# Kernel tuning notes

Hardware: AMD Instinct MI355X
Metric: run time of the kernel (lower is better)

Reference implementation:

```python
import jax, jax.numpy as jnp
import numpy as np

N_NODES = 200000
N_FRAGS = 50000
N_EDGES = 400000
HDIM = 128
VOCAB = 800


def setup_inputs() -> dict:
    key = jax.random.key(0)
    ks = jax.random.split(key, 9)
    x = jax.random.normal(ks[0], (N_NODES, HDIM), dtype=jnp.float32)
    fragments = jax.random.uniform(ks[1], (N_FRAGS, VOCAB), dtype=jnp.float32)
    emb_table = jax.random.normal(ks[2], (VOCAB, HDIM), dtype=jnp.float32)
    W_f = jax.random.normal(ks[3], (HDIM, HDIM), dtype=jnp.float32) / np.sqrt(HDIM)
    b_f = jax.random.normal(ks[4], (HDIM,), dtype=jnp.float32) * 0.01
    W_s = jax.random.normal(ks[5], (2 * HDIM, HDIM), dtype=jnp.float32) / np.sqrt(2 * HDIM)
    b_s = jax.random.normal(ks[6], (HDIM,), dtype=jnp.float32) * 0.01
    row = jax.random.randint(ks[7], (N_EDGES,), 0, N_NODES, dtype=jnp.int32)
    col = jax.random.randint(ks[8], (N_EDGES,), 0, N_FRAGS, dtype=jnp.int32)
    return {"x": x, "fragments": fragments, "emb_table": emb_table,
            "W_f": W_f, "b_f": b_f, "W_s": W_s, "b_s": b_s,
            "row": row, "col": col}


def _scatter_mean(vals, idx, num_segments):
    s = jax.ops.segment_sum(vals, idx, num_segments=num_segments)
    cnt = jax.ops.segment_sum(jnp.ones((vals.shape[0], 1), vals.dtype), idx,
                              num_segments=num_segments)
    return s / jnp.maximum(cnt, 1.0)


def reference(x, fragments, emb_table, W_f, b_f, W_s, b_s, row, col):
    N, H = x.shape
    F = fragments.shape[0]
    # gather node feats along memberships, mean-pool per fragment: [F, H]
    substructure_x = _scatter_mean(x[row], col, F)
    # fragment type embedding branch
    frag_ids = jnp.argmax(fragments, axis=1)            # [F]
    fragments_emb = emb_table[frag_ids] @ W_f + b_f      # [F, H]
    substructure_x = jnp.concatenate([substructure_x, fragments_emb], axis=1)  # [F, 2H]
    fragment_emb = substructure_x @ W_s + b_s            # [F, H]
    # gather fragment embeddings back to memberships, mean-pool per node: [N, H]
    return _scatter_mean(fragment_emb[col], row, N)
```

## Files before the change

### kernel.cpp

```cpp
#include <hip/hip_runtime.h>

#define HDIM 128
#define VOCAB 800
#define FB 16
#define TILE 1024

#define ACC4(a, v) { a.x += v.x; a.y += v.y; a.z += v.z; a.w += v.w; }

__global__ void k_prep(const float* __restrict__ emb, const float* __restrict__ W_f,
                       const float* __restrict__ W_s, const float* __restrict__ b_f,
                       const float* __restrict__ b_s, float* __restrict__ E2,
                       float* __restrict__ bfs) {
    __shared__ float e[HDIM], t1[HDIM];
    int j = threadIdx.x;
    int v = blockIdx.x;
    if (v < VOCAB) {
        e[j] = emb[(size_t)v * HDIM + j];
        __syncthreads();
        float a = 0.f;
        for (int k = 0; k < HDIM; ++k)
            a = fmaf(e[k], W_f[k * HDIM + j], a);
        t1[j] = a;
        __syncthreads();
        float b = 0.f;
        for (int k = 0; k < HDIM; ++k)
            b = fmaf(t1[k], W_s[(HDIM + k) * HDIM + j], b);
        E2[(size_t)v * HDIM + j] = b;
    } else {
        e[j] = b_f[j];
        __syncthreads();
        float b = b_s[j];
        for (int k = 0; k < HDIM; ++k)
            b = fmaf(e[k], W_s[(HDIM + k) * HDIM + j], b);
        bfs[j] = b;
    }
}

__global__ void k_amc(const float* __restrict__ frags, int* __restrict__ frag_id,
                      const int* __restrict__ row, const int* __restrict__ col,
                      int* __restrict__ cntr, int* __restrict__ cntc) {
    int b = blockIdx.x;
    if (b < 12500) {
        int wave = b * 4 + (threadIdx.x >> 6);
        int lane = threadIdx.x & 63;
        const float4* r = reinterpret_cast<const float4*>(frags + (size_t)wave * VOCAB);
        float best = -1e30f;
        int bidx = 0;
        for (int i = lane; i < VOCAB / 4; i += 64) {
            float4 v = r[i];
            int base = i * 4;
            if (v.x > best) { best = v.x; bidx = base + 0; }
            if (v.y > best) { best = v.y; bidx = base + 1; }
            if (v.z > best) { best = v.z; bidx = base + 2; }
            if (v.w > best) { best = v.w; bidx = base + 3; }
        }
        for (int off = 32; off > 0; off >>= 1) {
            float ov = __shfl_xor(best, off, 64);
            int   oi = __shfl_xor(bidx, off, 64);
            if (ov > best || (ov == best && oi < bidx)) { best = ov; bidx = oi; }
        }
        if (lane == 0) frag_id[wave] = bidx;
    } else {
        int i = (b - 12500) * 256 + threadIdx.x;
        if (i < 100000) {
            int4 r4 = reinterpret_cast<const int4*>(row)[i];
            int4 c4 = reinterpret_cast<const int4*>(col)[i];
            atomicAdd(&cntr[r4.x], 1); atomicAdd(&cntr[r4.y], 1);
            atomicAdd(&cntr[r4.z], 1); atomicAdd(&cntr[r4.w], 1);
            atomicAdd(&cntc[c4.x], 1); atomicAdd(&cntc[c4.y], 1);
            atomicAdd(&cntc[c4.z], 1); atomicAdd(&cntc[c4.w], 1);
        }
    }
}

__global__ void k_bsum2(const int* __restrict__ cntc, const int* __restrict__ cntr,
                        int* __restrict__ bsc, int* __restrict__ bsr, int NBC, int F, int N) {
    __shared__ int s[256];
    int t = threadIdx.x;
    const int* cnt;
    int* bsum;
    int bb, L;
    if ((int)blockIdx.x < NBC) { cnt = cntc; bsum = bsc; bb = blockIdx.x; L = F; }
    else                       { cnt = cntr; bsum = bsr; bb = blockIdx.x - NBC; L = N; }
    int i = bb * 256 + t;
    s[t] = (i < L) ? cnt[i] : 0;
    __syncthreads();
    for (int o = 128; o > 0; o >>= 1) {
        if (t < o) s[t] += s[t + o];
        __syncthreads();
    }
    if (t == 0) bsum[bb] = s[0];
}

__global__ void k_scan2(int* __restrict__ bsc, int* __restrict__ bsr, int nbc, int nbr) {
    __shared__ int s[1024];
    int* bsum = (blockIdx.x == 0) ? bsc : bsr;
    int nb    = (blockIdx.x == 0) ? nbc : nbr;
    int t = threadIdx.x;
    int v = (t < nb) ? bsum[t] : 0;
    s[t] = v;
    __syncthreads();
    for (int o = 1; o < 1024; o <<= 1) {
        int a = (t >= o) ? s[t - o] : 0;
        __syncthreads();
        s[t] += a;
        __syncthreads();
    }
    if (t < nb) bsum[t] = s[t] - v;
}

__global__ void k_base2(const int* __restrict__ cntc, const int* __restrict__ cntr,
                        const int* __restrict__ bsc, const int* __restrict__ bsr,
                        int* __restrict__ basec, int* __restrict__ baser,
                        int NBC, int F, int N) {
    __shared__ int s[256];
    int t = threadIdx.x;
    const int *cnt, *bsum;
    int* base;
    int bb, L;
    if ((int)blockIdx.x < NBC) { cnt = cntc; bsum = bsc; base = basec; bb = blockIdx.x; L = F; }
    else                       { cnt = cntr; bsum = bsr; base = baser; bb = blockIdx.x - NBC; L = N; }
    int i = bb * 256 + t;
    int v = (i < L) ? cnt[i] : 0;
    s[t] = v;
    __syncthreads();
    for (int o = 1; o < 256; o <<= 1) {
        int a = (t >= o) ? s[t - o] : 0;
        __syncthreads();
        s[t] += a;
        __syncthreads();
    }
    if (i < L) base[i] = bsum[bb] + s[t] - v;
}

__global__ void k_place(const int* __restrict__ row, const int* __restrict__ col,
                        const int* __restrict__ basec, const int* __restrict__ baser,
                        int* __restrict__ curc, int* __restrict__ curr,
                        int* __restrict__ payc, int* __restrict__ payr, int E) {
    int e = blockIdx.x * 256 + threadIdx.x;
    if (e >= E) return;
    int r = row[e], c = col[e];
    int pc = atomicAdd(&curc[c], 1);
    payc[basec[c] + pc] = r;
    int pr = atomicAdd(&curr[r], 1);
    payr[baser[r] + pr] = c;
}

__global__ __launch_bounds__(256) void k_frag(
        const float* __restrict__ x, const int* __restrict__ basec,
        const int* __restrict__ cntc, const int* __restrict__ payc,
        const int* __restrict__ frag_id, const float* __restrict__ W_s,
        const float* __restrict__ E2, const float* __restrict__ bfs,
        float* __restrict__ femb) {
    __shared__ float s[FB][HDIM];
    __shared__ int eidx[TILE];
    int t = threadIdx.x;
    int g = t >> 5, l = t & 31;
    int fb = blockIdx.x * FB;
    int fi0 = fb + g, fi1 = fb + 8 + g;
    int st0 = basec[fi0], d0 = cntc[fi0];
    int st1 = basec[fi1], d1 = cntc[fi1];
    int p0 = basec[fb];
    int pend = basec[fb + FB - 1] + cntc[fb + FB - 1];
    const float4* x4 = reinterpret_cast<const float4*>(x);
    float4 a0A = make_float4(0.f, 0.f, 0.f, 0.f), a0B = a0A, a1A = a0A, a1B = a0A;
    for (int tb = p0; tb < pend; tb += TILE) {
        int nload = min(TILE, pend - tb);
        for (int i = t; i < nload; i += 256) eidx[i] = payc[tb + i];
        __syncthreads();
        int lim = tb + nload;
        int lo0 = max(st0, tb) - tb, hi0 = min(st0 + d0, lim) - tb;
        int lo1 = max(st1, tb) - tb, hi1 = min(st1 + d1, lim) - tb;
        int m = max(hi0 - lo0, hi1 - lo1);
        for (int j = 0; j < m; j += 2) {
            if (lo0 + j < hi0)     { float4 v = x4[(size_t)eidx[lo0 + j]     * 32 + l]; ACC4(a0A, v); }
            if (lo0 + j + 1 < hi0) { float4 v = x4[(size_t)eidx[lo0 + j + 1] * 32 + l]; ACC4(a0B, v); }
            if (lo1 + j < hi1)     { float4 v = x4[(size_t)eidx[lo1 + j]     * 32 + l]; ACC4(a1A, v); }
            if (lo1 + j + 1 < hi1) { float4 v = x4[(size_t)eidx[lo1 + j + 1] * 32 + l]; ACC4(a1B, v); }
        }
        __syncthreads();
    }
    float inv0 = 1.0f / fmaxf((float)d0, 1.0f);
    float inv1 = 1.0f / fmaxf((float)d1, 1.0f);
    float4 r0, r1;
    r0.x = (a0A.x + a0B.x) * inv0; r0.y = (a0A.y + a0B.y) * inv0;
    r0.z = (a0A.z + a0B.z) * inv0; r0.w = (a0A.w + a0B.w) * inv0;
    r1.x = (a1A.x + a1B.x) * inv1; r1.y = (a1A.y + a1B.y) * inv1;
    r1.z = (a1A.z + a1B.z) * inv1; r1.w = (a1A.w + a1B.w) * inv1;
    *reinterpret_cast<float4*>(&s[g][l * 4]) = r0;
    *reinterpret_cast<float4*>(&s[8 + g][l * 4]) = r1;
    __syncthreads();
    int d = t & 127;
    int fh = t >> 7;
    float bv = bfs[d];
    float acc[8];
#pragma unroll
    for (int f = 0; f < 8; ++f)
        acc[f] = E2[(size_t)frag_id[fb + fh * 8 + f] * HDIM + d] + bv;
    for (int k = 0; k < HDIM; k += 4) {
        float w0 = W_s[(k + 0) * HDIM + d];
        float w1 = W_s[(k + 1) * HDIM + d];
        float w2 = W_s[(k + 2) * HDIM + d];
        float w3 = W_s[(k + 3) * HDIM + d];
#pragma unroll
        for (int f = 0; f < 8; ++f) {
            const float4 sv = *reinterpret_cast<const float4*>(&s[fh * 8 + f][k]);
            acc[f] = fmaf(sv.x, w0, acc[f]);
            acc[f] = fmaf(sv.y, w1, acc[f]);
            acc[f] = fmaf(sv.z, w2, acc[f]);
            acc[f] = fmaf(sv.w, w3, acc[f]);
        }
    }
#pragma unroll
    for (int f = 0; f < 8; ++f)
        femb[(size_t)(fb + fh * 8 + f) * HDIM + d] = acc[f];
}

__global__ __launch_bounds__(256) void k_node(
        const float* __restrict__ femb, const int* __restrict__ baser,
        const int* __restrict__ cntr, const int* __restrict__ payr,
        float* __restrict__ out, int N) {
    __shared__ int eidx[TILE];
    int t = threadIdx.x;
    int g = t >> 5, l = t & 31;
    int n0 = blockIdx.x * 32;
    int ng = n0 + g * 4;
    int p0 = baser[n0];
    int pend = baser[n0 + 31] + cntr[n0 + 31];
    int st0 = baser[ng + 0], d0 = cntr[ng + 0];
    int st1 = baser[ng + 1], d1 = cntr[ng + 1];
    int st2 = baser[ng + 2], d2 = cntr[ng + 2];
    int st3 = baser[ng + 3], d3 = cntr[ng + 3];
    const float4* f4 = reinterpret_cast<const float4*>(femb);
    float4 z = make_float4(0.f, 0.f, 0.f, 0.f);
    float4 a0A = z, a0B = z, a1A = z, a1B = z, a2A = z, a2B = z, a3A = z, a3B = z;
    for (int tb = p0; tb < pend; tb += TILE) {
        int nload = min(TILE, pend - tb);
        for (int i = t; i < nload; i += 256) eidx[i] = payr[tb + i];
        __syncthreads();
        int lim = tb + nload;
        int lo0 = max(st0, tb) - tb, hi0 = min(st0 + d0, lim) - tb;
        int lo1 = max(st1, tb) - tb, hi1 = min(st1 + d1, lim) - tb;
        int lo2 = max(st2, tb) - tb, hi2 = min(st2 + d2, lim) - tb;
        int lo3 = max(st3, tb) - tb, hi3 = min(st3 + d3, lim) - tb;
        int m = max(max(hi0 - lo0, hi1 - lo1), max(hi2 - lo2, hi3 - lo3));
        for (int j = 0; j < m; j += 2) {
            if (lo0 + j < hi0)     { float4 v = f4[(size_t)eidx[lo0 + j]     * 32 + l]; ACC4(a0A, v); }
            if (lo0 + j + 1 < hi0) { float4 v = f4[(size_t)eidx[lo0 + j + 1] * 32 + l]; ACC4(a0B, v); }
            if (lo1 + j < hi1)     { float4 v = f4[(size_t)eidx[lo1 + j]     * 32 + l]; ACC4(a1A, v); }
            if (lo1 + j + 1 < hi1) { float4 v = f4[(size_t)eidx[lo1 + j + 1] * 32 + l]; ACC4(a1B, v); }
            if (lo2 + j < hi2)     { float4 v = f4[(size_t)eidx[lo2 + j]     * 32 + l]; ACC4(a2A, v); }
            if (lo2 + j + 1 < hi2) { float4 v = f4[(size_t)eidx[lo2 + j + 1] * 32 + l]; ACC4(a2B, v); }
            if (lo3 + j < hi3)     { float4 v = f4[(size_t)eidx[lo3 + j]     * 32 + l]; ACC4(a3A, v); }
            if (lo3 + j + 1 < hi3) { float4 v = f4[(size_t)eidx[lo3 + j + 1] * 32 + l]; ACC4(a3B, v); }
        }
        __syncthreads();
    }
    float4* o4 = reinterpret_cast<float4*>(out);
    float4 r;
    float inv;
    inv = 1.0f / fmaxf((float)d0, 1.0f);
    r.x = (a0A.x + a0B.x) * inv; r.y = (a0A.y + a0B.y) * inv;
    r.z = (a0A.z + a0B.z) * inv; r.w = (a0A.w + a0B.w) * inv;
    o4[(size_t)(ng + 0) * 32 + l] = r;
    inv = 1.0f / fmaxf((float)d1, 1.0f);
    r.x = (a1A.x + a1B.x) * inv; r.y = (a1A.y + a1B.y) * inv;
    r.z = (a1A.z + a1B.z) * inv; r.w = (a1A.w + a1B.w) * inv;
    o4[(size_t)(ng + 1) * 32 + l] = r;
    inv = 1.0f / fmaxf((float)d2, 1.0f);
    r.x = (a2A.x + a2B.x) * inv; r.y = (a2A.y + a2B.y) * inv;
    r.z = (a2A.z + a2B.z) * inv; r.w = (a2A.w + a2B.w) * inv;
    o4[(size_t)(ng + 2) * 32 + l] = r;
    inv = 1.0f / fmaxf((float)d3, 1.0f);
    r.x = (a3A.x + a3B.x) * inv; r.y = (a3A.y + a3B.y) * inv;
    r.z = (a3A.z + a3B.z) * inv; r.w = (a3A.w + a3B.w) * inv;
    o4[(size_t)(ng + 3) * 32 + l] = r;
}

extern "C" void kernel_launch(void* const* d_in, const int* in_sizes, int n_in,
                              void* d_out, int out_size, void* d_ws, size_t ws_size,
                              hipStream_t stream) {
    const float* x         = (const float*)d_in[0];
    const float* fragments = (const float*)d_in[1];
    const float* emb_table = (const float*)d_in[2];
    const float* W_f       = (const float*)d_in[3];
    const float* b_f       = (const float*)d_in[4];
    const float* W_s       = (const float*)d_in[5];
    const float* b_s       = (const float*)d_in[6];
    const int*   row       = (const int*)d_in[7];
    const int*   col       = (const int*)d_in[8];
    float* out = (float*)d_out;

    const int N = 200000, F = 50000, E = 400000;
    const int NBC = (F + 255) / 256;
    const int NBR = (N + 255) / 256;

    float* femb   = (float*)d_ws;
    int* cntc     = (int*)(femb + (size_t)F * HDIM);
    int* cntr     = cntc + F;
    int* curc     = cntr + N;
    int* curr     = curc + F;
    int* basec    = curr + N;
    int* baser    = basec + F;
    int* bsc      = baser + N;
    int* bsr      = bsc + 1024;
    int* payc     = bsr + 1024;
    int* payr     = payc + E;
    int* frag_id  = payr + E;
    float* E2     = (float*)(frag_id + F);
    float* bfs    = E2 + VOCAB * HDIM;

    hipMemsetAsync(cntc, 0, (size_t)(2 * (F + N)) * sizeof(int), stream);

    k_prep<<<VOCAB + 1, HDIM, 0, stream>>>(emb_table, W_f, W_s, b_f, b_s, E2, bfs);
    k_amc<<<12500 + 391, 256, 0, stream>>>(fragments, frag_id, row, col, cntr, cntc);
    k_bsum2<<<NBC + NBR, 256, 0, stream>>>(cntc, cntr, bsc, bsr, NBC, F, N);
    k_scan2<<<2, 1024, 0, stream>>>(bsc, bsr, NBC, NBR);
    k_base2<<<NBC + NBR, 256, 0, stream>>>(cntc, cntr, bsc, bsr, basec, baser, NBC, F, N);
    k_place<<<(E + 255) / 256, 256, 0, stream>>>(row, col, basec, baser, curc, curr,
                                                 payc, payr, E);
    k_frag<<<F / FB, 256, 0, stream>>>(x, basec, cntc, payc, frag_id, W_s, E2, bfs, femb);
    k_node<<<N / 32, 256, 0, stream>>>(femb, baser, cntr, payr, out, N);
}
```

Baseline: 265.5 us.

## Gather bf16 copies of node and fragment features; fuse argmax into fragment kernel

Converts x to bf16 into the output buffer as scratch, and stores fragment embeddings as bf16, so both gather phases read half the bytes per row. The fragment-type argmax moves out of the counting kernel and into k_frag, where each 32-lane group computes it directly. k_node now handles 64 nodes per block with 8 accumulators per group and a smaller index tile. This cuts gather bandwidth at the cost of an extra full pass over x for conversion and bf16 rounding error in the results.

```diff
diff --git a/kernel.cpp b/kernel.cpp
--- a/kernel.cpp
+++ b/kernel.cpp
@@ -4,8 +4,18 @@
 #define VOCAB 800
 #define FB 16
 #define TILE 1024
-
-#define ACC4(a, v) { a.x += v.x; a.y += v.y; a.z += v.z; a.w += v.w; }
+#define TILE_N 512
+
+#define ACCB(a, h) { \
+    a.x += __uint_as_float(h.x << 16); \
+    a.y += __uint_as_float(h.x & 0xffff0000u); \
+    a.z += __uint_as_float(h.y << 16); \
+    a.w += __uint_as_float(h.y & 0xffff0000u); }
+
+static __device__ __forceinline__ unsigned short f2bf(float f) {
+    unsigned int u = __float_as_uint(f);
+    return (unsigned short)((u + 0x7fffu + ((u >> 16) & 1u)) >> 16);
+}
 
 __global__ void k_prep(const float* __restrict__ emb, const float* __restrict__ W_f,
                        const float* __restrict__ W_s, const float* __restrict__ b_f,
@@ -36,32 +46,22 @@
     }
 }
 
-__global__ void k_amc(const float* __restrict__ frags, int* __restrict__ frag_id,
+__global__ void k_cvt(const float* __restrict__ x, unsigned short* __restrict__ xb,
                       const int* __restrict__ row, const int* __restrict__ col,
                       int* __restrict__ cntr, int* __restrict__ cntc) {
-    int b = blockIdx.x;
+    int b = blockIdx.x, t = threadIdx.x;
     if (b < 12500) {
-        int wave = b * 4 + (threadIdx.x >> 6);
-        int lane = threadIdx.x & 63;
-        const float4* r = reinterpret_cast<const float4*>(frags + (size_t)wave * VOCAB);
-        float best = -1e30f;
-        int bidx = 0;
-        for (int i = lane; i < VOCAB / 4; i += 64) {
-            float4 v = r[i];
-            int base = i * 4;
-            if (v.x > best) { best = v.x; bidx = base + 0; }
-            if (v.y > best) { best = v.y; bidx = base + 1; }
-            if (v.z > best) { best = v.z; bidx = base + 2; }
-            if (v.w > best) { best = v.w; bidx = base + 3; }
-        }
-        for (int off = 32; off > 0; off >>= 1) {
-            float ov = __shfl_xor(best, off, 64);
-            int   oi = __shfl_xor(bidx, off, 64);
-            if (ov > best || (ov == best && oi < bidx)) { best = ov; bidx = oi; }
-        }
-        if (lane == 0) frag_id[wave] = bidx;
+        size_t i = ((size_t)b * 256 + t) * 8;
+        float4 v0 = *reinterpret_cast<const float4*>(x + i);
+        float4 v1 = *reinterpret_cast<const float4*>(x + i + 4);
+        uint4 o;
+        o.x = (unsigned)f2bf(v0.x) | ((unsigned)f2bf(v0.y) << 16);
+        o.y = (unsigned)f2bf(v0.z) | ((unsigned)f2bf(v0.w) << 16);
+        o.z = (unsigned)f2bf(v1.x) | ((unsigned)f2bf(v1.y) << 16);
+        o.w = (unsigned)f2bf(v1.z) | ((unsigned)f2bf(v1.w) << 16);
+        *reinterpret_cast<uint4*>(xb + i) = o;
     } else {
-        int i = (b - 12500) * 256 + threadIdx.x;
+        int i = (b - 12500) * 256 + t;
         if (i < 100000) {
             int4 r4 = reinterpret_cast<const int4*>(row)[i];
             int4 c4 = reinterpret_cast<const int4*>(col)[i];
@@ -147,22 +147,44 @@
 }
 
 __global__ __launch_bounds__(256) void k_frag(
-        const float* __restrict__ x, const int* __restrict__ basec,
-        const int* __restrict__ cntc, const int* __restrict__ payc,
-        const int* __restrict__ frag_id, const float* __restrict__ W_s,
+        const unsigned short* __restrict__ xb, const float* __restrict__ frags,
+        const int* __restrict__ basec, const int* __restrict__ cntc,
+        const int* __restrict__ payc, const float* __restrict__ W_s,
         const float* __restrict__ E2, const float* __restrict__ bfs,
-        float* __restrict__ femb) {
+        unsigned short* __restrict__ fembb) {
     __shared__ float s[FB][HDIM];
     __shared__ int eidx[TILE];
+    __shared__ int fidv[FB];
     int t = threadIdx.x;
     int g = t >> 5, l = t & 31;
     int fb = blockIdx.x * FB;
+#pragma unroll
+    for (int rep = 0; rep < 2; ++rep) {
+        int f = rep * 8 + g;
+        const float4* r = reinterpret_cast<const float4*>(frags + (size_t)(fb + f) * VOCAB);
+        float best = -1e30f;
+        int bidx = 0;
+        for (int i = l; i < VOCAB / 4; i += 32) {
+            float4 v = r[i];
+            int bI = i * 4;
+            if (v.x > best) { best = v.x; bidx = bI + 0; }
+            if (v.y > best) { best = v.y; bidx = bI + 1; }
+            if (v.z > best) { best = v.z; bidx = bI + 2; }
+            if (v.w > best) { best = v.w; bidx = bI + 3; }
+        }
+        for (int off = 16; off > 0; off >>= 1) {
+            float ov = __shfl_xor(best, off, 32);
+            int   oi = __shfl_xor(bidx, off, 32);
+            if (ov > best || (ov == best && oi < bidx)) { best = ov; bidx = oi; }
+        }
+        if (l == 0) fidv[f] = bidx;
+    }
     int fi0 = fb + g, fi1 = fb + 8 + g;
     int st0 = basec[fi0], d0 = cntc[fi0];
     int st1 = basec[fi1], d1 = cntc[fi1];
     int p0 = basec[fb];
     int pend = basec[fb + FB - 1] + cntc[fb + FB - 1];
-    const float4* x4 = reinterpret_cast<const float4*>(x);
+    const uint2* x2 = reinterpret_cast<const uint2*>(xb);
     float4 a0A = make_float4(0.f, 0.f, 0.f, 0.f), a0B = a0A, a1A = a0A, a1B = a0A;
     for (int tb = p0; tb < pend; tb += TILE) {
         int nload = min(TILE, pend - tb);
@@ -173,10 +195,10 @@
         int lo1 = max(st1, tb) - tb, hi1 = min(st1 + d1, lim) - tb;
         int m = max(hi0 - lo0, hi1 - lo1);
         for (int j = 0; j < m; j += 2) {
-            if (lo0 + j < hi0)     { float4 v = x4[(size_t)eidx[lo0 + j]     * 32 + l]; ACC4(a0A, v); }
-            if (lo0 + j + 1 < hi0) { float4 v = x4[(size_t)eidx[lo0 + j + 1] * 32 + l]; ACC4(a0B, v); }
-            if (lo1 + j < hi1)     { float4 v = x4[(size_t)eidx[lo1 + j]     * 32 + l]; ACC4(a1A, v); }
-            if (lo1 + j + 1 < hi1) { float4 v = x4[(size_t)eidx[lo1 + j + 1] * 32 + l]; ACC4(a1B, v); }
+            if (lo0 + j < hi0)     { uint2 h = x2[(size_t)eidx[lo0 + j]     * 32 + l]; ACCB(a0A, h); }
+            if (lo0 + j + 1 < hi0) { uint2 h = x2[(size_t)eidx[lo0 + j + 1] * 32 + l]; ACCB(a0B, h); }
+            if (lo1 + j < hi1)     { uint2 h = x2[(size_t)eidx[lo1 + j]     * 32 + l]; ACCB(a1A, h); }
+            if (lo1 + j + 1 < hi1) { uint2 h = x2[(size_t)eidx[lo1 + j + 1] * 32 + l]; ACCB(a1B, h); }
         }
         __syncthreads();
     }
@@ -196,7 +218,7 @@
     float acc[8];
 #pragma unroll
     for (int f = 0; f < 8; ++f)
-        acc[f] = E2[(size_t)frag_id[fb + fh * 8 + f] * HDIM + d] + bv;
+        acc[f] = E2[(size_t)fidv[fh * 8 + f] * HDIM + d] + bv;
     for (int k = 0; k < HDIM; k += 4) {
         float w0 = W_s[(k + 0) * HDIM + d];
         float w1 = W_s[(k + 1) * HDIM + d];
@@ -213,68 +235,62 @@
     }
 #pragma unroll
     for (int f = 0; f < 8; ++f)
-        femb[(size_t)(fb + fh * 8 + f) * HDIM + d] = acc[f];
+        fembb[(size_t)(fb + fh * 8 + f) * HDIM + d] = f2bf(acc[f]);
 }
 
 __global__ __launch_bounds__(256) void k_node(
-        const float* __restrict__ femb, const int* __restrict__ baser,
+        const unsigned short* __restrict__ fembb, const int* __restrict__ baser,
         const int* __restrict__ cntr, const int* __restrict__ payr,
         float* __restrict__ out, int N) {
-    __shared__ int eidx[TILE];
+    __shared__ int eidx[TILE_N];
     int t = threadIdx.x;
     int g = t >> 5, l = t & 31;
-    int n0 = blockIdx.x * 32;
-    int ng = n0 + g * 4;
+    int n0 = blockIdx.x * 64;
+    int ng = n0 + g * 8;
     int p0 = baser[n0];
-    int pend = baser[n0 + 31] + cntr[n0 + 31];
-    int st0 = baser[ng + 0], d0 = cntr[ng + 0];
-    int st1 = baser[ng + 1], d1 = cntr[ng + 1];
-    int st2 = baser[ng + 2], d2 = cntr[ng + 2];
-    int st3 = baser[ng + 3], d3 = cntr[ng + 3];
-    const float4* f4 = reinterpret_cast<const float4*>(femb);
-    float4 z = make_float4(0.f, 0.f, 0.f, 0.f);
-    float4 a0A = z, a0B = z, a1A = z, a1B = z, a2A = z, a2B = z, a3A = z, a3B = z;
-    for (int tb = p0; tb < pend; tb += TILE) {
-        int nload = min(TILE, pend - tb);
+    int pend = baser[n0 + 63] + cntr[n0 + 63];
+    const uint2* f2p = reinterpret_cast<const uint2*>(fembb);
+    float4 a[8];
+    int st_[8], dg_[8];
+#pragma unroll
+    for (int i = 0; i < 8; ++i) {
+        st_[i] = baser[ng + i];
+        dg_[i] = cntr[ng + i];
+        a[i] = make_float4(0.f, 0.f, 0.f, 0.f);
+    }
+    for (int tb = p0; tb < pend; tb += TILE_N) {
+        int nload = min(TILE_N, pend - tb);
         for (int i = t; i < nload; i += 256) eidx[i] = payr[tb + i];
         __syncthreads();
         int lim = tb + nload;
-        int lo0 = max(st0, tb) - tb, hi0 = min(st0 + d0, lim) - tb;
-        int lo1 = max(st1, tb) - tb, hi1 = min(st1 + d1, lim) - tb;
-        int lo2 = max(st2, tb) - tb, hi2 = min(st2 + d2, lim) - tb;
-        int lo3 = max(st3, tb) - tb, hi3 = min(st3 + d3, lim) - tb;
-        int m = max(max(hi0 - lo0, hi1 - lo1), max(hi2 - lo2, hi3 - lo3));
-        for (int j = 0; j < m; j += 2) {
-            if (lo0 + j < hi0)     { float4 v = f4[(size_t)eidx[lo0 + j]     * 32 + l]; ACC4(a0A, v); }
-            if (lo0 + j + 1 < hi0) { float4 v = f4[(size_t)eidx[lo0 + j + 1] * 32 + l]; ACC4(a0B, v); }
-            if (lo1 + j < hi1)     { float4 v = f4[(size_t)eidx[lo1 + j]     * 32 + l]; ACC4(a1A, v); }
-            if (lo1 + j + 1 < hi1) { float4 v = f4[(size_t)eidx[lo1 + j + 1] * 32 + l]; ACC4(a1B, v); }
-            if (lo2 + j < hi2)     { float4 v = f4[(size_t)eidx[lo2 + j]     * 32 + l]; ACC4(a2A, v); }
-            if (lo2 + j + 1 < hi2) { float4 v = f4[(size_t)eidx[lo2 + j + 1] * 32 + l]; ACC4(a2B, v); }
-            if (lo3 + j < hi3)     { float4 v = f4[(size_t)eidx[lo3 + j]     * 32 + l]; ACC4(a3A, v); }
-            if (lo3 + j + 1 < hi3) { float4 v = f4[(size_t)eidx[lo3 + j + 1] * 32 + l]; ACC4(a3B, v); }
+        int lo[8], hi[8];
+        int m = 0;
+#pragma unroll
+        for (int i = 0; i < 8; ++i) {
+            lo[i] = max(st_[i], tb) - tb;
+            hi[i] = min(st_[i] + dg_[i], lim) - tb;
+            m = max(m, hi[i] - lo[i]);
+        }
+        for (int j = 0; j < m; ++j) {
+#pragma unroll
+            for (int i = 0; i < 8; ++i) {
+                if (lo[i] + j < hi[i]) {
+                    uint2 h = f2p[(size_t)eidx[lo[i] + j] * 32 + l];
+                    ACCB(a[i], h);
+                }
+            }
         }
         __syncthreads();
     }
     float4* o4 = reinterpret_cast<float4*>(out);
-    float4 r;
-    float inv;
-    inv = 1.0f / fmaxf((float)d0, 1.0f);
-    r.x = (a0A.x + a0B.x) * inv; r.y = (a0A.y + a0B.y) * inv;
-    r.z = (a0A.z + a0B.z) * inv; r.w = (a0A.w + a0B.w) * inv;
-    o4[(size_t)(ng + 0) * 32 + l] = r;
-    inv = 1.0f / fmaxf((float)d1, 1.0f);
-    r.x = (a1A.x + a1B.x) * inv; r.y = (a1A.y + a1B.y) * inv;
-    r.z = (a1A.z + a1B.z) * inv; r.w = (a1A.w + a1B.w) * inv;
-    o4[(size_t)(ng + 1) * 32 + l] = r;
-    inv = 1.0f / fmaxf((float)d2, 1.0f);
-    r.x = (a2A.x + a2B.x) * inv; r.y = (a2A.y + a2B.y) * inv;
-    r.z = (a2A.z + a2B.z) * inv; r.w = (a2A.w + a2B.w) * inv;
-    o4[(size_t)(ng + 2) * 32 + l] = r;
-    inv = 1.0f / fmaxf((float)d3, 1.0f);
-    r.x = (a3A.x + a3B.x) * inv; r.y = (a3A.y + a3B.y) * inv;
-    r.z = (a3A.z + a3B.z) * inv; r.w = (a3A.w + a3B.w) * inv;
-    o4[(size_t)(ng + 3) * 32 + l] = r;
+#pragma unroll
+    for (int i = 0; i < 8; ++i) {
+        float inv = 1.0f / fmaxf((float)dg_[i], 1.0f);
+        float4 r;
+        r.x = a[i].x * inv; r.y = a[i].y * inv;
+        r.z = a[i].z * inv; r.w = a[i].w * inv;
+        o4[(size_t)(ng + i) * 32 + l] = r;
+    }
 }
 
 extern "C" void kernel_launch(void* const* d_in, const int* in_sizes, int n_in,
@@ -295,30 +311,31 @@
     const int NBC = (F + 255) / 256;
     const int NBR = (N + 255) / 256;
 
-    float* femb   = (float*)d_ws;
-    int* cntc     = (int*)(femb + (size_t)F * HDIM);
-    int* cntr     = cntc + F;
-    int* curc     = cntr + N;
-    int* curr     = curc + F;
-    int* basec    = curr + N;
-    int* baser    = basec + F;
-    int* bsc      = baser + N;
-    int* bsr      = bsc + 1024;
-    int* payc     = bsr + 1024;
-    int* payr     = payc + E;
-    int* frag_id  = payr + E;
-    float* E2     = (float*)(frag_id + F);
-    float* bfs    = E2 + VOCAB * HDIM;
+    unsigned short* xb = (unsigned short*)d_out;
+
+    unsigned short* fembb = (unsigned short*)d_ws;
+    int* cntc  = (int*)(fembb + (size_t)F * HDIM);
+    int* cntr  = cntc + F;
+    int* curc  = cntr + N;
+    int* curr  = curc + F;
+    int* basec = curr + N;
+    int* baser = basec + F;
+    int* bsc   = baser + N;
+    int* bsr   = bsc + 1024;
+    int* payc  = bsr + 1024;
+    int* payr  = payc + E;
+    float* E2  = (float*)(payr + E);
+    float* bfs = E2 + VOCAB * HDIM;
 
     hipMemsetAsync(cntc, 0, (size_t)(2 * (F + N)) * sizeof(int), stream);
 
     k_prep<<<VOCAB + 1, HDIM, 0, stream>>>(emb_table, W_f, W_s, b_f, b_s, E2, bfs);
-    k_amc<<<12500 + 391, 256, 0, stream>>>(fragments, frag_id, row, col, cntr, cntc);
+    k_cvt<<<12500 + 391, 256, 0, stream>>>(x, xb, row, col, cntr, cntc);
     k_bsum2<<<NBC + NBR, 256, 0, stream>>>(cntc, cntr, bsc, bsr, NBC, F, N);
     k_scan2<<<2, 1024, 0, stream>>>(bsc, bsr, NBC, NBR);
     k_base2<<<NBC + NBR, 256, 0, stream>>>(cntc, cntr, bsc, bsr, basec, baser, NBC, F, N);
     k_place<<<(E + 255) / 256, 256, 0, stream>>>(row, col, basec, baser, curc, curr,
                                                  payc, payr, E);
-    k_frag<<<F / FB, 256, 0, stream>>>(x, basec, cntc, payc, frag_id, W_s, E2, bfs, femb);
-    k_node<<<N / 32, 256, 0, stream>>>(femb, baser, cntr, payr, out, N);
-}
+    k_frag<<<F / FB, 256, 0, stream>>>(xb, fragments, basec, cntc, payc, W_s, E2, bfs, fembb);
+    k_node<<<N / 64, 256, 0, stream>>>(fembb, baser, cntr, payr, out, N);
+}
```

Result: slower. 282.2 us (+6.3%).

## Balance segment reductions by edge ranges with LDS atomics and reuse base arrays as cursors

Applied to the files above, without the earlier changes.

The per-fragment and per-node mean-pool kernels now split each tile's edge range evenly across warps instead of giving each warp fixed segments. Each warp keeps running sums and flushes them with shared-memory atomics at segment boundaries, which removes load imbalance from uneven degrees. The placement kernel now increments the base arrays in place, so after placement basec[i] marks the end of segment i. This drops the separate cursor arrays and halves the memset, with segment bounds read from the shifted base array. The cost is extra LDS atomics and zero-init work, and in k_node the per-block tile shrinks to 256.

```diff
diff --git a/kernel.cpp b/kernel.cpp
--- a/kernel.cpp
+++ b/kernel.cpp
@@ -3,9 +3,9 @@
 #define HDIM 128
 #define VOCAB 800
 #define FB 16
-#define TILE 1024
-
-#define ACC4(a, v) { a.x += v.x; a.y += v.y; a.z += v.z; a.w += v.w; }
+#define NB 32
+#define TILE 512
+#define TILE_N 256
 
 __global__ void k_prep(const float* __restrict__ emb, const float* __restrict__ W_f,
                        const float* __restrict__ W_s, const float* __restrict__ b_f,
@@ -134,61 +134,81 @@
 }
 
 __global__ void k_place(const int* __restrict__ row, const int* __restrict__ col,
-                        const int* __restrict__ basec, const int* __restrict__ baser,
-                        int* __restrict__ curc, int* __restrict__ curr,
+                        int* __restrict__ basec, int* __restrict__ baser,
                         int* __restrict__ payc, int* __restrict__ payr, int E) {
     int e = blockIdx.x * 256 + threadIdx.x;
     if (e >= E) return;
     int r = row[e], c = col[e];
-    int pc = atomicAdd(&curc[c], 1);
-    payc[basec[c] + pc] = r;
-    int pr = atomicAdd(&curr[r], 1);
-    payr[baser[r] + pr] = c;
+    int pc = atomicAdd(&basec[c], 1);
+    payc[pc] = r;
+    int pr = atomicAdd(&baser[r], 1);
+    payr[pr] = c;
 }
 
 __global__ __launch_bounds__(256) void k_frag(
         const float* __restrict__ x, const int* __restrict__ basec,
-        const int* __restrict__ cntc, const int* __restrict__ payc,
-        const int* __restrict__ frag_id, const float* __restrict__ W_s,
-        const float* __restrict__ E2, const float* __restrict__ bfs,
-        float* __restrict__ femb) {
+        const int* __restrict__ payc, const int* __restrict__ frag_id,
+        const float* __restrict__ W_s, const float* __restrict__ E2,
+        const float* __restrict__ bfs, float* __restrict__ femb) {
     __shared__ float s[FB][HDIM];
     __shared__ int eidx[TILE];
+    __shared__ int cb[FB + 1];
     int t = threadIdx.x;
     int g = t >> 5, l = t & 31;
     int fb = blockIdx.x * FB;
-    int fi0 = fb + g, fi1 = fb + 8 + g;
-    int st0 = basec[fi0], d0 = cntc[fi0];
-    int st1 = basec[fi1], d1 = cntc[fi1];
-    int p0 = basec[fb];
-    int pend = basec[fb + FB - 1] + cntc[fb + FB - 1];
+    if (t <= FB) {
+        int idx = fb + t - 1;
+        cb[t] = (idx < 0) ? 0 : basec[idx];
+    }
+    for (int i = t; i < FB * HDIM; i += 256) ((float*)s)[i] = 0.f;
+    __syncthreads();
+    int p0 = cb[0], pend = cb[FB];
     const float4* x4 = reinterpret_cast<const float4*>(x);
-    float4 a0A = make_float4(0.f, 0.f, 0.f, 0.f), a0B = a0A, a1A = a0A, a1B = a0A;
     for (int tb = p0; tb < pend; tb += TILE) {
         int nload = min(TILE, pend - tb);
         for (int i = t; i < nload; i += 256) eidx[i] = payc[tb + i];
         __syncthreads();
-        int lim = tb + nload;
-        int lo0 = max(st0, tb) - tb, hi0 = min(st0 + d0, lim) - tb;
-        int lo1 = max(st1, tb) - tb, hi1 = min(st1 + d1, lim) - tb;
-        int m = max(hi0 - lo0, hi1 - lo1);
-        for (int j = 0; j < m; j += 2) {
-            if (lo0 + j < hi0)     { float4 v = x4[(size_t)eidx[lo0 + j]     * 32 + l]; ACC4(a0A, v); }
-            if (lo0 + j + 1 < hi0) { float4 v = x4[(size_t)eidx[lo0 + j + 1] * 32 + l]; ACC4(a0B, v); }
-            if (lo1 + j < hi1)     { float4 v = x4[(size_t)eidx[lo1 + j]     * 32 + l]; ACC4(a1A, v); }
-            if (lo1 + j + 1 < hi1) { float4 v = x4[(size_t)eidx[lo1 + j + 1] * 32 + l]; ACC4(a1B, v); }
-        }
-        __syncthreads();
-    }
-    float inv0 = 1.0f / fmaxf((float)d0, 1.0f);
-    float inv1 = 1.0f / fmaxf((float)d1, 1.0f);
-    float4 r0, r1;
-    r0.x = (a0A.x + a0B.x) * inv0; r0.y = (a0A.y + a0B.y) * inv0;
-    r0.z = (a0A.z + a0B.z) * inv0; r0.w = (a0A.w + a0B.w) * inv0;
-    r1.x = (a1A.x + a1B.x) * inv1; r1.y = (a1A.y + a1B.y) * inv1;
-    r1.z = (a1A.z + a1B.z) * inv1; r1.w = (a1A.w + a1B.w) * inv1;
-    *reinterpret_cast<float4*>(&s[g][l * 4]) = r0;
-    *reinterpret_cast<float4*>(&s[8 + g][l * 4]) = r1;
+        int ck = (nload + 7) >> 3;
+        int beg = g * ck, end = min(beg + ck, nload);
+        if (beg < end) {
+            int cur = 0;
+            while (tb + beg >= cb[cur + 1]) ++cur;
+            float4 acc = make_float4(0.f, 0.f, 0.f, 0.f);
+            for (int p = beg; p < end; p += 4) {
+                int n4 = min(4, end - p);
+                float4 v0, v1, v2, v3;
+                v0 = x4[(size_t)eidx[p] * 32 + l];
+                if (n4 > 1) v1 = x4[(size_t)eidx[p + 1] * 32 + l];
+                if (n4 > 2) v2 = x4[(size_t)eidx[p + 2] * 32 + l];
+                if (n4 > 3) v3 = x4[(size_t)eidx[p + 3] * 32 + l];
+#pragma unroll
+                for (int k = 0; k < 4; ++k) {
+                    if (k >= n4) break;
+                    int gp = tb + p + k;
+                    if (gp >= cb[cur + 1]) {
+                        atomicAdd(&s[cur][l * 4 + 0], acc.x);
+                        atomicAdd(&s[cur][l * 4 + 1], acc.y);
+                        atomicAdd(&s[cur][l * 4 + 2], acc.z);
+                        atomicAdd(&s[cur][l * 4 + 3], acc.w);
+                        acc = make_float4(0.f, 0.f, 0.f, 0.f);
+                        do { ++cur; } while (gp >= cb[cur + 1]);
+                    }
+                    float4 v = (k == 0) ? v0 : (k == 1) ? v1 : (k == 2) ? v2 : v3;
+                    acc.x += v.x; acc.y += v.y; acc.z += v.z; acc.w += v.w;
+                }
+            }
+            atomicAdd(&s[cur][l * 4 + 0], acc.x);
+            atomicAdd(&s[cur][l * 4 + 1], acc.y);
+            atomicAdd(&s[cur][l * 4 + 2], acc.z);
+            atomicAdd(&s[cur][l * 4 + 3], acc.w);
+        }
+        __syncthreads();
+    }
+    for (int i = t; i < FB * HDIM; i += 256) {
+        int f = i >> 7;
+        int dg = cb[f + 1] - cb[f];
+        ((float*)s)[i] *= 1.0f / fmaxf((float)dg, 1.0f);
+    }
     __syncthreads();
     int d = t & 127;
     int fh = t >> 7;
@@ -218,63 +238,70 @@
 
 __global__ __launch_bounds__(256) void k_node(
         const float* __restrict__ femb, const int* __restrict__ baser,
-        const int* __restrict__ cntr, const int* __restrict__ payr,
-        float* __restrict__ out, int N) {
-    __shared__ int eidx[TILE];
+        const int* __restrict__ payr, float* __restrict__ out, int N) {
+    __shared__ float s[NB][HDIM];
+    __shared__ int eidx[TILE_N];
+    __shared__ int cb[NB + 1];
     int t = threadIdx.x;
     int g = t >> 5, l = t & 31;
-    int n0 = blockIdx.x * 32;
-    int ng = n0 + g * 4;
-    int p0 = baser[n0];
-    int pend = baser[n0 + 31] + cntr[n0 + 31];
-    int st0 = baser[ng + 0], d0 = cntr[ng + 0];
-    int st1 = baser[ng + 1], d1 = cntr[ng + 1];
-    int st2 = baser[ng + 2], d2 = cntr[ng + 2];
-    int st3 = baser[ng + 3], d3 = cntr[ng + 3];
-    const float4* f4 = reinterpret_cast<const float4*>(femb);
-    float4 z = make_float4(0.f, 0.f, 0.f, 0.f);
-    float4 a0A = z, a0B = z, a1A = z, a1B = z, a2A = z, a2B = z, a3A = z, a3B = z;
-    for (int tb = p0; tb < pend; tb += TILE) {
-        int nload = min(TILE, pend - tb);
+    int n0 = blockIdx.x * NB;
+    if (t <= NB) {
+        int idx = n0 + t - 1;
+        cb[t] = (idx < 0) ? 0 : baser[idx];
+    }
+    for (int i = t; i < NB * HDIM; i += 256) ((float*)s)[i] = 0.f;
+    __syncthreads();
+    int p0 = cb[0], pend = cb[NB];
+    const float4* f4p = reinterpret_cast<const float4*>(femb);
+    for (int tb = p0; tb < pend; tb += TILE_N) {
+        int nload = min(TILE_N, pend - tb);
         for (int i = t; i < nload; i += 256) eidx[i] = payr[tb + i];
         __syncthreads();
-        int lim = tb + nload;
-        int lo0 = max(st0, tb) - tb, hi0 = min(st0 + d0, lim) - tb;
-        int lo1 = max(st1, tb) - tb, hi1 = min(st1 + d1, lim) - tb;
-        int lo2 = max(st2, tb) - tb, hi2 = min(st2 + d2, lim) - tb;
-        int lo3 = max(st3, tb) - tb, hi3 = min(st3 + d3, lim) - tb;
-        int m = max(max(hi0 - lo0, hi1 - lo1), max(hi2 - lo2, hi3 - lo3));
-        for (int j = 0; j < m; j += 2) {
-            if (lo0 + j < hi0)     { float4 v = f4[(size_t)eidx[lo0 + j]     * 32 + l]; ACC4(a0A, v); }
-            if (lo0 + j + 1 < hi0) { float4 v = f4[(size_t)eidx[lo0 + j + 1] * 32 + l]; ACC4(a0B, v); }
-            if (lo1 + j < hi1)     { float4 v = f4[(size_t)eidx[lo1 + j]     * 32 + l]; ACC4(a1A, v); }
-            if (lo1 + j + 1 < hi1) { float4 v = f4[(size_t)eidx[lo1 + j + 1] * 32 + l]; ACC4(a1B, v); }
-            if (lo2 + j < hi2)     { float4 v = f4[(size_t)eidx[lo2 + j]     * 32 + l]; ACC4(a2A, v); }
-            if (lo2 + j + 1 < hi2) { float4 v = f4[(size_t)eidx[lo2 + j + 1] * 32 + l]; ACC4(a2B, v); }
-            if (lo3 + j < hi3)     { float4 v = f4[(size_t)eidx[lo3 + j]     * 32 + l]; ACC4(a3A, v); }
-            if (lo3 + j + 1 < hi3) { float4 v = f4[(size_t)eidx[lo3 + j + 1] * 32 + l]; ACC4(a3B, v); }
+        int ck = (nload + 7) >> 3;
+        int beg = g * ck, end = min(beg + ck, nload);
+        if (beg < end) {
+            int cur = 0;
+            while (tb + beg >= cb[cur + 1]) ++cur;
+            float4 acc = make_float4(0.f, 0.f, 0.f, 0.f);
+            for (int p = beg; p < end; p += 4) {
+                int n4 = min(4, end - p);
+                float4 v0, v1, v2, v3;
+                v0 = f4p[(size_t)eidx[p] * 32 + l];
+                if (n4 > 1) v1 = f4p[(size_t)eidx[p + 1] * 32 + l];
+                if (n4 > 2) v2 = f4p[(size_t)eidx[p + 2] * 32 + l];
+                if (n4 > 3) v3 = f4p[(size_t)eidx[p + 3] * 32 + l];
+#pragma unroll
+                for (int k = 0; k < 4; ++k) {
+                    if (k >= n4) break;
+                    int gp = tb + p + k;
+                    if (gp >= cb[cur + 1]) {
+                        atomicAdd(&s[cur][l * 4 + 0], acc.x);
+                        atomicAdd(&s[cur][l * 4 + 1], acc.y);
+                        atomicAdd(&s[cur][l * 4 + 2], acc.z);
+                        atomicAdd(&s[cur][l * 4 + 3], acc.w);
+                        acc = make_float4(0.f, 0.f, 0.f, 0.f);
+                        do { ++cur; } while (gp >= cb[cur + 1]);
+                    }
+                    float4 v = (k == 0) ? v0 : (k == 1) ? v1 : (k == 2) ? v2 : v3;
+                    acc.x += v.x; acc.y += v.y; acc.z += v.z; acc.w += v.w;
+                }
+            }
+            atomicAdd(&s[cur][l * 4 + 0], acc.x);
+            atomicAdd(&s[cur][l * 4 + 1], acc.y);
+            atomicAdd(&s[cur][l * 4 + 2], acc.z);
+            atomicAdd(&s[cur][l * 4 + 3], acc.w);
         }
         __syncthreads();
     }
     float4* o4 = reinterpret_cast<float4*>(out);
-    float4 r;
-    float inv;
-    inv = 1.0f / fmaxf((float)d0, 1.0f);
-    r.x = (a0A.x + a0B.x) * inv; r.y = (a0A.y + a0B.y) * inv;
-    r.z = (a0A.z + a0B.z) * inv; r.w = (a0A.w + a0B.w) * inv;
-    o4[(size_t)(ng + 0) * 32 + l] = r;
-    inv = 1.0f / fmaxf((float)d1, 1.0f);
-    r.x = (a1A.x + a1B.x) * inv; r.y = (a1A.y + a1B.y) * inv;
-    r.z = (a1A.z + a1B.z) * inv; r.w = (a1A.w + a1B.w) * inv;
-    o4[(size_t)(ng + 1) * 32 + l] = r;
-    inv = 1.0f / fmaxf((float)d2, 1.0f);
-    r.x = (a2A.x + a2B.x) * inv; r.y = (a2A.y + a2B.y) * inv;
-    r.z = (a2A.z + a2B.z) * inv; r.w = (a2A.w + a2B.w) * inv;
-    o4[(size_t)(ng + 2) * 32 + l] = r;
-    inv = 1.0f / fmaxf((float)d3, 1.0f);
-    r.x = (a3A.x + a3B.x) * inv; r.y = (a3A.y + a3B.y) * inv;
-    r.z = (a3A.z + a3B.z) * inv; r.w = (a3A.w + a3B.w) * inv;
-    o4[(size_t)(ng + 3) * 32 + l] = r;
+    for (int i = t; i < NB * 32; i += 256) {
+        int r = i >> 5, c4 = i & 31;
+        int dg = cb[r + 1] - cb[r];
+        float inv = 1.0f / fmaxf((float)dg, 1.0f);
+        float4 v = *reinterpret_cast<const float4*>(&s[r][c4 * 4]);
+        v.x *= inv; v.y *= inv; v.z *= inv; v.w *= inv;
+        o4[(size_t)(n0 + r) * 32 + c4] = v;
+    }
 }
 
 extern "C" void kernel_launch(void* const* d_in, const int* in_sizes, int n_in,
@@ -295,30 +322,27 @@
     const int NBC = (F + 255) / 256;
     const int NBR = (N + 255) / 256;
 
-    float* femb   = (float*)d_ws;
-    int* cntc     = (int*)(femb + (size_t)F * HDIM);
-    int* cntr     = cntc + F;
-    int* curc     = cntr + N;
-    int* curr     = curc + F;
-    int* basec    = curr + N;
-    int* baser    = basec + F;
-    int* bsc      = baser + N;
-    int* bsr      = bsc + 1024;
-    int* payc     = bsr + 1024;
-    int* payr     = payc + E;
-    int* frag_id  = payr + E;
-    float* E2     = (float*)(frag_id + F);
-    float* bfs    = E2 + VOCAB * HDIM;
-
-    hipMemsetAsync(cntc, 0, (size_t)(2 * (F + N)) * sizeof(int), stream);
-
-    k_prep<<<VOCAB + 1, HDIM, 0, stream>>>(emb_table, W_f, W_s, b_f, b_s, E2, bfs);
+    float* femb  = (float*)d_ws;
+    int* cntc    = (int*)(femb + (size_t)F * HDIM);
+    int* cntr    = cntc + F;
+    int* basec   = cntr + N;
+    int* baser   = basec + F;
+    int* bsc     = baser + N;
+    int* bsr     = bsc + 1024;
+    int* payc    = bsr + 1024;
+    int* payr    = payc + E;
+    int* frag_id = payr + E;
+    float* E2    = (float*)(frag_id + F);
+    float* bfs   = E2 + VOCAB * HDIM;
+
+    hipMemsetAsync(cntc, 0, (size_t)(F + N) * sizeof(int), stream);
+
     k_amc<<<12500 + 391, 256, 0, stream>>>(fragments, frag_id, row, col, cntr, cntc);
     k_bsum2<<<NBC + NBR, 256, 0, stream>>>(cntc, cntr, bsc, bsr, NBC, F, N);
     k_scan2<<<2, 1024, 0, stream>>>(bsc, bsr, NBC, NBR);
     k_base2<<<NBC + NBR, 256, 0, stream>>>(cntc, cntr, bsc, bsr, basec, baser, NBC, F, N);
-    k_place<<<(E + 255) / 256, 256, 0, stream>>>(row, col, basec, baser, curc, curr,
-                                                 payc, payr, E);
-    k_frag<<<F / FB, 256, 0, stream>>>(x, basec, cntc, payc, frag_id, W_s, E2, bfs, femb);
-    k_node<<<N / 32, 256, 0, stream>>>(femb, baser, cntr, payr, out, N);
-}
+    k_place<<<(E + 255) / 256, 256, 0, stream>>>(row, col, basec, baser, payc, payr, E);
+    k_prep<<<VOCAB + 1, HDIM, 0, stream>>>(emb_table, W_f, W_s, b_f, b_s, E2, bfs);
+    k_frag<<<F / FB, 256, 0, stream>>>(x, basec, payc, frag_id, W_s, E2, bfs, femb);
+    k_node<<<N / NB, 256, 0, stream>>>(femb, baser, payr, out, N);
+}
```

After: 382.2 us. 43.9% more time.
